# Optimization experiments

Measured on AMD Instinct MI355X. Metric: run time of the kernel, lower is better.

The kernel has to match this reference:

```python
import jax, jax.numpy as jnp
import numpy as np

B = 2048   # batch of sampled occupation configurations
L = 64     # nphysical (spatial orbitals / MPS sites)
P = 4      # local physical dimension (2 spin orbitals -> 4 occupations)
D = 128    # MPS bond dimension


def setup_inputs() -> dict:
    key = jax.random.key(0)
    k1, k2, k3, k4 = jax.random.split(key, 4)
    onstate = jax.random.randint(k1, (B, L), 0, P)  # occupation per site
    # flat MPS data buffer reshaped to [site, occupation, Dl, Dr];
    # scale by D**-0.5 so the length-L matrix chain stays O(1).
    site_tensors = jax.random.normal(k2, (L, P, D, D), dtype=jnp.float32) * (D ** -0.5)
    left_vec = jax.random.normal(k3, (D,), dtype=jnp.float32)
    right_vec = jax.random.normal(k4, (D,), dtype=jnp.float32)
    return {
        "onstate": onstate,
        "site_tensors": site_tensors,
        "left_vec": left_vec,
        "right_vec": right_vec,
    }


def reference(onstate, site_tensors, right_vec, left_vec=None, **_ignore):
    # keyword-robust shim not needed; real signature below
    raise NotImplementedError


def reference(onstate, site_tensors, left_vec, right_vec):
    """MPS amplitude: amp[b] = l^T (prod_i A[i, s_{b,i}]) r, evaluated as a
    left-to-right chain of gathered batched vector-matrix products."""
    batch = onstate.shape[0]
    s_seq = onstate.T.astype(jnp.int32)                      # [L, B]
    v0 = jnp.broadcast_to(left_vec, (batch, left_vec.shape[0]))  # [B, D]

    def step(v, inp):
        A_i, s_i = inp            # A_i: [P, D, D], s_i: [B]
        M = A_i[s_i]              # data-dependent gather -> [B, D, D]
        v = jnp.einsum('bd,bde->be', v, M)
        return v, None

    vL, _ = jax.lax.scan(step, v0, (site_tensors, s_seq))
    return vL @ right_vec         # [B] amplitudes
```

## Files before the change

kernel.cpp:

```cpp
#include <hip/hip_runtime.h>
#include <hip/hip_fp16.h>

constexpr int L = 64;
constexpr int P = 4;
constexpr int D = 128;
constexpr int B = 2048;
constexpr int EPW = 16;
constexpr int NG = B / EPW;

using v8h = __attribute__((ext_vector_type(8))) _Float16;
using v4f = __attribute__((ext_vector_type(4))) float;

constexpr size_t UT_OFF  = 0;
constexpr size_t WT_OFF  = 1048576;
constexpr size_t MTF_OFF = 2097152;
constexpr size_t MTB_OFF = 6291456;

#define WAIT_LGKM0 0xC07F

__global__ void convert_dual(const float* __restrict__ src,
                             _Float16* __restrict__ mtf,
                             _Float16* __restrict__ mtb) {
  const int mat  = blockIdx.x >> 1;
  const int half = blockIdx.x & 1;
  const int site = mat >> 2, p = mat & 3;
  const int wave = threadIdx.x >> 6, lane = threadIdx.x & 63;
  const int me = lane & 15, q4 = lane >> 4;
  const float* sb = src + (size_t)mat * 16384;

  if (site >= 32) {
    _Float16* ob = mtb + (size_t)(site - 32) * 65536 + p * 16384;
#pragma unroll
    for (int i = 0; i < 4; ++i) {
      const int kh = half * 2 + (i >> 1);
      const int w  = (i & 1) * 4 + wave;
      const float4* rp =
          (const float4*)(sb + (w * 16 + me) * 128 + (kh * 4 + q4) * 8);
      float4 f0 = rp[0], f1 = rp[1];
      v8h v = {(_Float16)f0.x, (_Float16)f0.y, (_Float16)f0.z, (_Float16)f0.w,
               (_Float16)f1.x, (_Float16)f1.y, (_Float16)f1.z, (_Float16)f1.w};
      *(v8h*)(ob + kh * 4096 + w * 512 + q4 * 128 + me * 8) = v;
    }
    return;
  }
  _Float16* ob = mtf + (size_t)site * 65536 + p * 16384;
#pragma unroll
  for (int i = 0; i < 4; ++i) {
    const int kh = half * 2 + (i >> 1);
    const int w  = (i & 1) * 4 + wave;
    v8h v;
#pragma unroll
    for (int j = 0; j < 8; ++j)
      v[j] = (_Float16)sb[((kh * 4 + q4) * 8 + j) * 128 + w * 16 + me];
    *(v8h*)(ob + kh * 4096 + w * 512 + q4 * 128 + me * 8) = v;
  }
}

__global__ __launch_bounds__(512, 2) void mps_half_chain(
    const int* __restrict__ onstate, const _Float16* __restrict__ mtf,
    const _Float16* __restrict__ mtb, const float* __restrict__ left_vec,
    const float* __restrict__ right_vec, float* __restrict__ ut,
    float* __restrict__ wt) {
  __shared__ _Float16 vlds[2][2048];
  __shared__ int plds[L * EPW];
  const int tid = threadIdx.x;
  const int wave = tid >> 6, lane = tid & 63;
  const int me = lane & 15, q4 = lane >> 4;
  const bool fwd = !(blockIdx.x & 1);
  const int b0 = (blockIdx.x >> 1) * EPW;
  const _Float16* mbase = fwd ? mtf : mtb;
  const float* ivec = fwd ? left_vec : right_vec;
  float* ovec = fwd ? ut : wt;

#pragma unroll
  for (int j = 0; j < 2; ++j) {
    int idx = tid + j * 512;
    int e = idx >> 6, i = idx & 63;
    plds[i * EPW + e] = onstate[(b0 + e) * L + i];
  }
  if (tid < 256) {
    int e = tid >> 4, seg = tid & 15;
    _Float16* vp = &vlds[0][0] + e * 128 + (seg ^ (e & 7)) * 8;
#pragma unroll
    for (int j = 0; j < 8; ++j) vp[j] = (_Float16)ivec[seg * 8 + j];
  }

  const _Float16* gbase = mbase + wave * 512 + lane * 8;
  auto stageR = [&](v8h (&bank)[16], int ls) {
    const v8h* gp = (const v8h*)(gbase + (size_t)ls * 65536);
#pragma unroll
    for (int i = 0; i < 16; ++i) bank[i] = gp[i * 512];
  };
  auto consumeSite = [&](v8h (&bank)[16], int pm, const _Float16* vb,
                         v4f& acc) {
    v8h a0 = *(const v8h*)(vb + me * 128 + ((q4) ^ (me & 7)) * 8);
    v8h a1 = *(const v8h*)(vb + me * 128 + ((q4 + 4) ^ (me & 7)) * 8);
    v8h a2 = *(const v8h*)(vb + me * 128 + ((q4 + 8) ^ (me & 7)) * 8);
    v8h a3 = *(const v8h*)(vb + me * 128 + ((q4 + 12) ^ (me & 7)) * 8);
    v4f c00 = {0.f, 0.f, 0.f, 0.f}, c01 = {0.f, 0.f, 0.f, 0.f};
    v4f c10 = {0.f, 0.f, 0.f, 0.f}, c11 = {0.f, 0.f, 0.f, 0.f};
#pragma unroll
    for (int p = 0; p < P; ++p) {
      const bool isp = (pm == p);
      v8h zf = {};
      v8h m0 = isp ? a0 : zf;
      v8h m1 = isp ? a1 : zf;
      v8h m2 = isp ? a2 : zf;
      v8h m3 = isp ? a3 : zf;
      v4f& cA = (p < 2) ? c00 : c01;
      v4f& cB = (p < 2) ? c10 : c11;
      cA = __builtin_amdgcn_mfma_f32_16x16x32_f16(m0, bank[p * 4 + 0], cA,
                                                  0, 0, 0);
      cA = __builtin_amdgcn_mfma_f32_16x16x32_f16(m1, bank[p * 4 + 1], cA,
                                                  0, 0, 0);
      cB = __builtin_amdgcn_mfma_f32_16x16x32_f16(m2, bank[p * 4 + 2], cB,
                                                  0, 0, 0);
      cB = __builtin_amdgcn_mfma_f32_16x16x32_f16(m3, bank[p * 4 + 3], cB,
                                                  0, 0, 0);
    }
    acc = acc + ((c00 + c01) + (c10 + c11));
  };
  const int c0 = wave * 16 + me;
  auto writeV = [&](_Float16* vn, const v4f& acc) {
#pragma unroll
    for (int r = 0; r < 4; ++r) {
      int e = q4 * 4 + r;
      vn[e * 128 + ((c0 >> 3) ^ (e & 7)) * 8 + (c0 & 7)] = (_Float16)acc[r];
    }
  };

  __syncthreads();

  v8h bank0[16], bank1[16];
  stageR(bank0, fwd ? 0 : 31);

  v4f accL = {0.f, 0.f, 0.f, 0.f};
  for (int s2 = 0; s2 < 16; ++s2) {
    const int se = 2 * s2, so = se + 1;
    {
      const int sg = fwd ? se : 63 - se;
      const int pm = plds[sg * EPW + me];
      stageR(bank1, fwd ? so : 31 - so);
      v4f acc = {0.f, 0.f, 0.f, 0.f};
      consumeSite(bank0, pm, &vlds[0][0], acc);
      writeV(&vlds[1][0], acc);
      __builtin_amdgcn_sched_barrier(0);
      __builtin_amdgcn_s_waitcnt(WAIT_LGKM0);
      __builtin_amdgcn_s_barrier();
      __builtin_amdgcn_sched_barrier(0);
    }
    {
      const int sg = fwd ? so : 63 - so;
      const int pm = plds[sg * EPW + me];
      const int sn = (so + 1) & 31;
      stageR(bank0, fwd ? sn : 31 - sn);
      v4f acc = {0.f, 0.f, 0.f, 0.f};
      consumeSite(bank1, pm, &vlds[1][0], acc);
      if (so < 31) {
        writeV(&vlds[0][0], acc);
        __builtin_amdgcn_sched_barrier(0);
        __builtin_amdgcn_s_waitcnt(WAIT_LGKM0);
        __builtin_amdgcn_s_barrier();
        __builtin_amdgcn_sched_barrier(0);
      } else {
        accL = acc;
      }
    }
  }
#pragma unroll
  for (int r = 0; r < 4; ++r) ovec[c0 * B + b0 + q4 * 4 + r] = accL[r];
}

__global__ void combine_uw(const float* __restrict__ ut,
                           const float* __restrict__ wt,
                           float* __restrict__ out) {
  __shared__ float red[256];
  const int t = threadIdx.x;
  const int b = blockIdx.x * 64 + (t & 63);
  const int w = t >> 6;
  float s = 0.f;
#pragma unroll
  for (int i = 0; i < 32; ++i) {
    const int d = w * 32 + i;
    s += ut[d * B + b] * wt[d * B + b];
  }
  red[t] = s;
  __syncthreads();
  if (t < 64) out[b] = red[t] + red[t + 64] + red[t + 128] + red[t + 192];
}

extern "C" void kernel_launch(void* const* d_in, const int* in_sizes, int n_in,
                              void* d_out, int out_size, void* d_ws,
                              size_t ws_size, hipStream_t stream) {
  const int*   onstate      = (const int*)d_in[0];
  const float* site_tensors = (const float*)d_in[1];
  const float* left_vec     = (const float*)d_in[2];
  const float* right_vec    = (const float*)d_in[3];
  float*       out          = (float*)d_out;
  char*        ws           = (char*)d_ws;
  float*       ut           = (float*)(ws + UT_OFF);
  float*       wt           = (float*)(ws + WT_OFF);
  _Float16*    mtf          = (_Float16*)(ws + MTF_OFF);
  _Float16*    mtb          = (_Float16*)(ws + MTB_OFF);

  convert_dual<<<L * P * 2, 256, 0, stream>>>(site_tensors, mtf, mtb);
  mps_half_chain<<<2 * NG, 512, 0, stream>>>(
      onstate, mtf, mtb, left_vec, right_vec, ut, wt);
  combine_uw<<<B / 64, 256, 0, stream>>>(ut, wt, out);
}
```

Measured before the change: 115.8 us.

## Fuse combine into half-chain kernel via last-arriver atomic flag

Measured after the change: 228.1 us. 1.97x slower.

```diff
diff --git a/kernel.cpp b/kernel.cpp
--- a/kernel.cpp
+++ b/kernel.cpp
@@ -15,12 +15,15 @@
 constexpr size_t WT_OFF  = 1048576;
 constexpr size_t MTF_OFF = 2097152;
 constexpr size_t MTB_OFF = 6291456;
+constexpr size_t FLG_OFF = 10485760;
 
 #define WAIT_LGKM0 0xC07F
 
 __global__ void convert_dual(const float* __restrict__ src,
                              _Float16* __restrict__ mtf,
-                             _Float16* __restrict__ mtb) {
+                             _Float16* __restrict__ mtb,
+                             int* __restrict__ flags) {
+  if (blockIdx.x == 0 && threadIdx.x < NG) flags[threadIdx.x] = 0;
   const int mat  = blockIdx.x >> 1;
   const int half = blockIdx.x & 1;
   const int site = mat >> 2, p = mat & 3;
@@ -60,14 +63,17 @@
     const int* __restrict__ onstate, const _Float16* __restrict__ mtf,
     const _Float16* __restrict__ mtb, const float* __restrict__ left_vec,
     const float* __restrict__ right_vec, float* __restrict__ ut,
-    float* __restrict__ wt) {
+    float* __restrict__ wt, int* __restrict__ flags,
+    float* __restrict__ out) {
   __shared__ _Float16 vlds[2][2048];
   __shared__ int plds[L * EPW];
+  __shared__ int who;
   const int tid = threadIdx.x;
   const int wave = tid >> 6, lane = tid & 63;
   const int me = lane & 15, q4 = lane >> 4;
   const bool fwd = !(blockIdx.x & 1);
-  const int b0 = (blockIdx.x >> 1) * EPW;
+  const int grp = blockIdx.x >> 1;
+  const int b0 = grp * EPW;
   const _Float16* mbase = fwd ? mtf : mtb;
   const float* ivec = fwd ? left_vec : right_vec;
   float* ovec = fwd ? ut : wt;
@@ -89,7 +95,8 @@
   auto stageR = [&](v8h (&bank)[16], int ls) {
     const v8h* gp = (const v8h*)(gbase + (size_t)ls * 65536);
 #pragma unroll
-    for (int i = 0; i < 16; ++i) bank[i] = gp[i * 512];
+    for (int i = 0; i < 16; ++i)
+      bank[i] = __builtin_nontemporal_load(&gp[i * 512]);
   };
   auto consumeSite = [&](v8h (&bank)[16], int pm, const _Float16* vb,
                          v4f& acc) {
@@ -128,21 +135,23 @@
       vn[e * 128 + ((c0 >> 3) ^ (e & 7)) * 8 + (c0 & 7)] = (_Float16)acc[r];
     }
   };
+  auto lsOf = [&](int s) { return fwd ? s : 31 - s; };
+  auto sgOf = [&](int s) { return fwd ? s : 63 - s; };
 
   __syncthreads();
 
   v8h bank0[16], bank1[16];
-  stageR(bank0, fwd ? 0 : 31);
-
+  stageR(bank0, lsOf(0));
+
+  int pm = plds[sgOf(0) * EPW + me];
   v4f accL = {0.f, 0.f, 0.f, 0.f};
   for (int s2 = 0; s2 < 16; ++s2) {
     const int se = 2 * s2, so = se + 1;
     {
-      const int sg = fwd ? se : 63 - se;
-      const int pm = plds[sg * EPW + me];
-      stageR(bank1, fwd ? so : 31 - so);
+      stageR(bank1, lsOf(so));
       v4f acc = {0.f, 0.f, 0.f, 0.f};
       consumeSite(bank0, pm, &vlds[0][0], acc);
+      pm = plds[sgOf(so) * EPW + me];
       writeV(&vlds[1][0], acc);
       __builtin_amdgcn_sched_barrier(0);
       __builtin_amdgcn_s_waitcnt(WAIT_LGKM0);
@@ -150,13 +159,11 @@
       __builtin_amdgcn_sched_barrier(0);
     }
     {
-      const int sg = fwd ? so : 63 - so;
-      const int pm = plds[sg * EPW + me];
-      const int sn = (so + 1) & 31;
-      stageR(bank0, fwd ? sn : 31 - sn);
+      if (so < 31) stageR(bank0, lsOf(so + 1));
       v4f acc = {0.f, 0.f, 0.f, 0.f};
       consumeSite(bank1, pm, &vlds[1][0], acc);
       if (so < 31) {
+        pm = plds[sgOf(so + 1) * EPW + me];
         writeV(&vlds[0][0], acc);
         __builtin_amdgcn_sched_barrier(0);
         __builtin_amdgcn_s_waitcnt(WAIT_LGKM0);
@@ -169,24 +176,21 @@
   }
 #pragma unroll
   for (int r = 0; r < 4; ++r) ovec[c0 * B + b0 + q4 * 4 + r] = accL[r];
-}
-
-__global__ void combine_uw(const float* __restrict__ ut,
-                           const float* __restrict__ wt,
-                           float* __restrict__ out) {
-  __shared__ float red[256];
-  const int t = threadIdx.x;
-  const int b = blockIdx.x * 64 + (t & 63);
-  const int w = t >> 6;
+
+  __threadfence();
+  __syncthreads();
+  if (tid == 0) who = atomicAdd(&flags[grp], 1);
+  __syncthreads();
+  if (who == 0) return;
+  __threadfence();
+  const int b = b0 + (tid >> 5);
+  const int dg = (tid & 31) * 4;
   float s = 0.f;
 #pragma unroll
-  for (int i = 0; i < 32; ++i) {
-    const int d = w * 32 + i;
-    s += ut[d * B + b] * wt[d * B + b];
-  }
-  red[t] = s;
-  __syncthreads();
-  if (t < 64) out[b] = red[t] + red[t + 64] + red[t + 128] + red[t + 192];
+  for (int i = 0; i < 4; ++i) s += ut[(dg + i) * B + b] * wt[(dg + i) * B + b];
+#pragma unroll
+  for (int o = 16; o; o >>= 1) s += __shfl_down(s, o, 32);
+  if ((tid & 31) == 0) out[b] = s;
 }
 
 extern "C" void kernel_launch(void* const* d_in, const int* in_sizes, int n_in,
@@ -202,9 +206,9 @@
   float*       wt           = (float*)(ws + WT_OFF);
   _Float16*    mtf          = (_Float16*)(ws + MTF_OFF);
   _Float16*    mtb          = (_Float16*)(ws + MTB_OFF);
-
-  convert_dual<<<L * P * 2, 256, 0, stream>>>(site_tensors, mtf, mtb);
+  int*         flags        = (int*)(ws + FLG_OFF);
+
+  convert_dual<<<L * P * 2, 256, 0, stream>>>(site_tensors, mtf, mtb, flags);
   mps_half_chain<<<2 * NG, 512, 0, stream>>>(
-      onstate, mtf, mtb, left_vec, right_vec, ut, wt);
-  combine_uw<<<B / 64, 256, 0, stream>>>(ut, wt, out);
+      onstate, mtf, mtb, left_vec, right_vec, ut, wt, flags, out);
 }
```
